# Kernel optimization log

Measured on AMD Instinct MI355X. Metric: run time of the kernel, lower is better.

The kernel has to match this reference:

```python
import jax, jax.numpy as jnp
import numpy as np

B, S, D = 1, 8192, 1024
H, HD = 16, 64
WIN = 1024      # sliding_window_size
CHUNK = 1024    # chunk_size
OVERLAP = 128   # chunk_overlap


def setup_inputs() -> dict:
    key = jax.random.key(0)
    ks = jax.random.split(key, 5)
    s = 1.0 / np.sqrt(D)
    inp = {"x": jax.random.normal(ks[0], (B, S, D), jnp.float32)}
    for i, n in enumerate(["Wq", "Wk", "Wv", "Wo"]):
        inp[n] = jax.random.normal(ks[1 + i], (D, D), jnp.float32) * s
    for n in ["bq", "bk", "bv", "bo"]:
        inp[n] = jnp.zeros((D,), jnp.float32)
    return inp


def _attend_chunk(q, k, v, chunk_start, win_start):
    # q: [B, Lq, H, HD]; k, v: [B, Lk, H, HD]
    Lq, Lk = q.shape[1], k.shape[1]
    q_abs = chunk_start + jnp.arange(Lq)[:, None]   # absolute query positions
    k_abs = win_start + jnp.arange(Lk)[None, :]     # absolute key positions
    allowed = (k_abs >= q_abs - WIN // 2) & (k_abs < q_abs + WIN // 2)
    scale = 1.0 / np.sqrt(HD)
    scores = jnp.einsum('bqhd,bkhd->bhqk', q, k) * scale  # [B,H,Lq,Lk]
    scores = jnp.where(allowed[None, None], scores, -jnp.inf)
    p = jax.nn.softmax(scores, axis=-1)
    return jnp.einsum('bhqk,bkhd->bqhd', p, v)


def _overlap_weight(cs, ce):
    # replicate torch linspace overlap-add blend weights (host-side constants)
    w = np.ones(ce - cs, np.float32)
    if cs > 0:
        n = min(cs + OVERLAP, ce) - cs
        w[:n] = np.linspace(0.0, 1.0, n, dtype=np.float32)
    if ce < S:
        os_ = max(cs, ce - OVERLAP)
        w[os_ - cs:] = np.linspace(1.0, 0.0, ce - os_, dtype=np.float32)
    return jnp.asarray(w)


def reference(x, Wq, bq, Wk, bk, Wv, bv, Wo, bo):
    q = (x @ Wq.T + bq).reshape(B, S, H, HD)
    k = (x @ Wk.T + bk).reshape(B, S, H, HD)
    v = (x @ Wv.T + bv).reshape(B, S, H, HD)
    out = jnp.zeros((B, S, H, HD), x.dtype)
    step = CHUNK - OVERLAP
    for cs in range(0, S, step):  # static Python loop over ~10 chunks
        ce = min(cs + CHUNK, S)
        ws, we = max(0, cs - WIN // 2), min(S, ce + WIN // 2)
        o = _attend_chunk(q[:, cs:ce], k[:, ws:we], v[:, ws:we], cs, ws)
        w = _overlap_weight(cs, ce)
        out = out.at[:, cs:ce].add(o * w[None, :, None, None])
    out = out.reshape(B, S, D)
    return out @ Wo.T + bo
```

## Files before the change

kernel.cpp:

```cpp
#include <hip/hip_runtime.h>

#define DEVI __device__ __forceinline__

constexpr int S = 8192, D = 1024, H = 16, HD = 64;
constexpr int NQKV = 3 * D;

typedef __attribute__((ext_vector_type(8))) __bf16 bf16x8;
typedef __attribute__((ext_vector_type(8))) unsigned short us8;
typedef __attribute__((ext_vector_type(4))) float f32x4;

DEVI unsigned short f2b(float f) {
  unsigned int u = __float_as_uint(f);
  u += 0x7fff + ((u >> 16) & 1);
  return (unsigned short)(u >> 16);
}

DEVI ushort4 cvt4(float4 v) {
  ushort4 r; r.x = f2b(v.x); r.y = f2b(v.y); r.z = f2b(v.z); r.w = f2b(v.w); return r;
}

DEVI void load_lds16(const void* g, void* l) {
  __builtin_amdgcn_global_load_lds((const __attribute__((address_space(1))) void*)g,
                                   (__attribute__((address_space(3))) void*)l,
                                   16, 0, 0);
}

__global__ void prep_kernel(const float4* __restrict__ x,
                            const float4* __restrict__ Wq, const float4* __restrict__ Wk,
                            const float4* __restrict__ Wv, const float4* __restrict__ Wo,
                            const float4* __restrict__ bq, const float4* __restrict__ bk,
                            const float4* __restrict__ bv,
                            ushort4* __restrict__ xb, ushort4* __restrict__ wqkv,
                            ushort4* __restrict__ wob, float4* __restrict__ biasq)
{
  constexpr int NX = S * D / 4;
  constexpr int NW = D * D / 4;
  constexpr int NB = D / 4;
  constexpr int TOT = NX + 4 * NW + 3 * NB;
  for (int i = blockIdx.x * blockDim.x + threadIdx.x; i < TOT; i += gridDim.x * blockDim.x) {
    if (i < NX) {
      xb[i] = cvt4(x[i]);
    } else if (i < NX + 3 * NW) {
      int j = i - NX;
      const float4* src = (j < NW) ? Wq : ((j < 2 * NW) ? Wk : Wv);
      int jj = (j < NW) ? j : ((j < 2 * NW) ? j - NW : j - 2 * NW);
      wqkv[j] = cvt4(src[jj]);
    } else if (i < NX + 4 * NW) {
      int j = i - NX - 3 * NW;
      wob[j] = cvt4(Wo[j]);
    } else {
      int j = i - NX - 4 * NW;
      const float4* src = (j < NB) ? bq : ((j < 2 * NB) ? bk : bv);
      int jj = (j < NB) ? j : ((j < 2 * NB) ? j - NB : j - 2 * NB);
      biasq[j] = src[jj];
    }
  }
}

template<int LDC, bool OUT_BF16>
__global__ __launch_bounds__(256)
void gemm_nt(const unsigned short* __restrict__ A,
             const unsigned short* __restrict__ B,
             const float* __restrict__ bias,
             void* __restrict__ C, int K)
{
  __shared__ __align__(16) unsigned short As[128 * 32];
  __shared__ __align__(16) unsigned short Bs[128 * 32];
  const int tid = threadIdx.x;
  const int wave = tid >> 6, lane = tid & 63;
  const int quad = lane >> 4, l15 = lane & 15;
  const int m0 = blockIdx.x * 128, n0 = blockIdx.y * 128;
  const int wr = wave >> 1, wc = wave & 1;

  const f32x4 fzero = {0.f, 0.f, 0.f, 0.f};
  f32x4 acc[4][4];
#pragma unroll
  for (int i = 0; i < 4; ++i)
#pragma unroll
    for (int j = 0; j < 4; ++j) acc[i][j] = fzero;

  const int segr = lane >> 2;
  const int cpst = lane & 3;

  for (int k0 = 0; k0 < K; k0 += 32) {
    __syncthreads();
#pragma unroll
    for (int j = 0; j < 4; ++j) {
      const int s = wave * 4 + j;
      const int s7 = s & 7;
      const int r = s7 * 16 + segr;
      const int c = cpst ^ ((r >> 1) & 3);
      const unsigned short* g = (s < 8)
        ? A + (size_t)(m0 + r) * K + k0 + c * 8
        : B + (size_t)(n0 + r) * K + k0 + c * 8;
      unsigned short* l = ((s < 8) ? As : Bs) + s7 * 512;
      load_lds16(g, l);
    }
    __syncthreads();

    bf16x8 af[4], bfr[4];
#pragma unroll
    for (int it = 0; it < 4; ++it) {
      const int r = wr * 64 + it * 16 + l15;
      const int cp = quad ^ ((r >> 1) & 3);
      af[it] = *(const bf16x8*)&As[r * 32 + cp * 8];
    }
#pragma unroll
    for (int jt = 0; jt < 4; ++jt) {
      const int r = wc * 64 + jt * 16 + l15;
      const int cp = quad ^ ((r >> 1) & 3);
      bfr[jt] = *(const bf16x8*)&Bs[r * 32 + cp * 8];
    }
#pragma unroll
    for (int it = 0; it < 4; ++it)
#pragma unroll
      for (int jt = 0; jt < 4; ++jt)
        acc[it][jt] = __builtin_amdgcn_mfma_f32_16x16x32_bf16(af[it], bfr[jt], acc[it][jt], 0, 0, 0);
  }

#pragma unroll
  for (int it = 0; it < 4; ++it)
#pragma unroll
    for (int jt = 0; jt < 4; ++jt) {
      const int col = n0 + wc * 64 + jt * 16 + l15;
      const float bv = bias[col];
#pragma unroll
      for (int i = 0; i < 4; ++i) {
        const int row = m0 + wr * 64 + it * 16 + quad * 4 + i;
        const float v = acc[it][jt][i] + bv;
        if constexpr (OUT_BF16)
          ((unsigned short*)C)[(size_t)row * LDC + col] = f2b(v);
        else
          ((float*)C)[(size_t)row * LDC + col] = v;
      }
    }
}

__global__ __launch_bounds__(256)
void attn_fused(const unsigned short* __restrict__ qkv,
                unsigned short* __restrict__ attnb)
{
  __shared__ __align__(16) unsigned short Ks[2][64 * 64];
  __shared__ __align__(16) unsigned short Vt[2][64 * 72];
  __shared__ __align__(16) unsigned short Ps[4][16 * 72];
  const int tid = threadIdx.x;
  const int wave = tid >> 6, lane = tid & 63;
  const int quad = lane >> 4, l15 = lane & 15;
  const int h = blockIdx.y;
  const int q0 = blockIdx.x * 128;
  const int wq0 = q0 + wave * 32;

  const unsigned short* Qp = qkv + h * HD;
  const unsigned short* Kp = qkv + D + h * HD;
  const unsigned short* Vp = qkv + 2 * D + h * HD;

  bf16x8 qf[2][2];
#pragma unroll
  for (int rt = 0; rt < 2; ++rt)
#pragma unroll
    for (int ksp = 0; ksp < 2; ++ksp)
      qf[rt][ksp] = *(const bf16x8*)(Qp + (size_t)(wq0 + rt * 16 + l15) * NQKV + ksp * 32 + quad * 8);

  const f32x4 fzero = {0.f, 0.f, 0.f, 0.f};
  f32x4 o[2][4];
  float lr[2][4];
#pragma unroll
  for (int rt = 0; rt < 2; ++rt)
#pragma unroll
    for (int i = 0; i < 4; ++i) { o[rt][i] = fzero; lr[rt][i] = 0.f; }

  const int ks = (q0 >= 512) ? (q0 - 512) : 0;
  const int ke = (q0 + 640 < S) ? (q0 + 640) : S;

  const int skey = tid >> 3;
  const int sg   = tid & 7;
  const int kdc  = sg ^ (skey & 7);

  us8 vreg[2];

#define STAGE_K(kt_, b_)                                                          \
  {                                                                               \
    _Pragma("unroll")                                                             \
    for (int r = 0; r < 2; ++r)                                                   \
      load_lds16(Kp + (size_t)((kt_) + skey + r * 32) * NQKV + kdc * 8,           \
                 &Ks[b_][(size_t)tid * 8 + r * 2048]);                            \
  }
#define LOAD_V(kt_)                                                               \
  {                                                                               \
    _Pragma("unroll")                                                             \
    for (int r = 0; r < 2; ++r)                                                   \
      vreg[r] = *(const us8*)(Vp + (size_t)((kt_) + skey + r * 32) * NQKV + sg * 8); \
  }
#define SCAT_V(b_)                                                                \
  {                                                                               \
    _Pragma("unroll")                                                             \
    for (int r = 0; r < 2; ++r) {                                                 \
      const int key = skey + r * 32;                                              \
      const int ch = (key >> 3) ^ sg;                                             \
      unsigned short* dst = &Vt[b_][sg * 8 * 72 + ch * 8 + (key & 7)];            \
      _Pragma("unroll")                                                           \
      for (int j = 0; j < 8; ++j) dst[j * 72] = vreg[r][j];                       \
    }                                                                             \
  }

  STAGE_K(ks, 0);
  LOAD_V(ks);
  SCAT_V(0);

  int b = 0;
  for (int kt = ks; kt < ke; kt += 64, b ^= 1) {
    __syncthreads();
    const int nx = kt + 64;
    const bool more = (nx < ke);
    if (more) { STAGE_K(nx, b ^ 1); LOAD_V(nx); }

    if (kt + 63 >= wq0 - 512 && kt <= wq0 + 542) {
      unsigned short* Pw = (unsigned short*)Ps[wave];
#pragma unroll
      for (int st = 0; st < 2; ++st) {
        const int C0 = kt + st * 32;
        if (!((C0 + 31 >= wq0 - 512) && (C0 <= wq0 + 16 + 526))) continue;

        bf16x8 kf[2][2];
#pragma unroll
        for (int hh2 = 0; hh2 < 2; ++hh2)
#pragma unroll
          for (int ksp = 0; ksp < 2; ++ksp)
            kf[hh2][ksp] = *(const bf16x8*)&Ks[b][((st * 2 + hh2) * 16 + l15) * 64
                                                  + ((ksp * 4 + quad) ^ (l15 & 7)) * 8];
        bf16x8 vf[4];
#pragma unroll
        for (int vt = 0; vt < 4; ++vt) {
          const int d = vt * 16 + l15;
          vf[vt] = *(const bf16x8*)&Vt[b][d * 72 + (((st * 4 + quad) ^ (d >> 3)) & 7) * 8];
        }

#pragma unroll
        for (int rt = 0; rt < 2; ++rt) {
          const int R = wq0 + rt * 16;
          if (!((C0 + 31 >= R - 512) && (C0 <= R + 526))) continue;

#pragma unroll
          for (int hh2 = 0; hh2 < 2; ++hh2) {
            const int C = C0 + hh2 * 16;
            const bool any  = (C + 15 >= R - 512) && (C <= R + 526);
            const bool full = (C >= R - 497) && (C <= R + 496);
            float p[4];
            if (!any) {
              p[0] = p[1] = p[2] = p[3] = 0.f;
            } else {
              f32x4 z = fzero;
              z = __builtin_amdgcn_mfma_f32_16x16x32_bf16(qf[rt][0], kf[hh2][0], z, 0, 0, 0);
              z = __builtin_amdgcn_mfma_f32_16x16x32_bf16(qf[rt][1], kf[hh2][1], z, 0, 0, 0);
              if (full) {
#pragma unroll
                for (int i = 0; i < 4; ++i) p[i] = __expf(z[i] * 0.125f);
              } else {
#pragma unroll
                for (int i = 0; i < 4; ++i) {
                  const int qa = R + quad * 4 + i;
                  const int ka = C + l15;
                  const unsigned u = (unsigned)(ka - qa + 512);
                  p[i] = (u < 1024u) ? __expf(z[i] * 0.125f) : 0.f;
                }
              }
            }
#pragma unroll
            for (int i = 0; i < 4; ++i) {
              lr[rt][i] += p[i];
              Pw[(quad * 4 + i) * 72 + st * 32 + hh2 * 16 + l15] = f2b(p[i]);
            }
          }
          asm volatile("s_waitcnt lgkmcnt(0)" ::: "memory");

          const bf16x8 pf = *(const bf16x8*)&Pw[l15 * 72 + (st * 4 + quad) * 8];
#pragma unroll
          for (int vt = 0; vt < 4; ++vt)
            o[rt][vt] = __builtin_amdgcn_mfma_f32_16x16x32_bf16(pf, vf[vt], o[rt][vt], 0, 0, 0);
        }
      }
    }

    if (more) SCAT_V(b ^ 1);
  }

#pragma unroll
  for (int rt = 0; rt < 2; ++rt)
#pragma unroll
    for (int i = 0; i < 4; ++i) {
      float l = lr[rt][i];
#pragma unroll
      for (int dd = 1; dd < 16; dd <<= 1) l += __shfl_xor(l, dd);
      const int qa = wq0 + rt * 16 + quad * 4 + i;
      const float w = (qa >= S - 128) ? (1.0f + (float)(qa - (S - 128)) * (1.0f / 127.0f)) : 1.0f;
      const float scl = w / l;
#pragma unroll
      for (int vt = 0; vt < 4; ++vt)
        attnb[(size_t)qa * D + h * HD + vt * 16 + l15] = f2b(o[rt][vt][i] * scl);
    }
#undef STAGE_K
#undef LOAD_V
#undef SCAT_V
}

extern "C" void kernel_launch(void* const* d_in, const int* in_sizes, int n_in,
                              void* d_out, int out_size, void* d_ws, size_t ws_size,
                              hipStream_t stream)
{
  const float* x  = (const float*)d_in[0];
  const float* Wq = (const float*)d_in[1];
  const float* Wk = (const float*)d_in[2];
  const float* Wv = (const float*)d_in[3];
  const float* Wo = (const float*)d_in[4];
  const float* bq = (const float*)d_in[5];
  const float* bk = (const float*)d_in[6];
  const float* bv = (const float*)d_in[7];
  const float* bo = (const float*)d_in[8];

  char* ws = (char*)d_ws;
  unsigned short* xb    = (unsigned short*)(ws);
  unsigned short* wqkv  = (unsigned short*)(ws + 16777216);
  unsigned short* wob   = (unsigned short*)(ws + 23068672);
  float*          biasq = (float*)         (ws + 25165824);
  unsigned short* qkv   = (unsigned short*)(ws + 25178112);
  unsigned short* attnb = (unsigned short*)(ws + 75509760);

  prep_kernel<<<2048, 256, 0, stream>>>((const float4*)x, (const float4*)Wq, (const float4*)Wk,
                                        (const float4*)Wv, (const float4*)Wo, (const float4*)bq,
                                        (const float4*)bk, (const float4*)bv,
                                        (ushort4*)xb, (ushort4*)wqkv, (ushort4*)wob, (float4*)biasq);

  gemm_nt<NQKV, true><<<dim3(64, 24), 256, 0, stream>>>(xb, wqkv, biasq, (void*)qkv, D);
  attn_fused<<<dim3(S / 128, H), 256, 0, stream>>>(qkv, attnb);
  gemm_nt<D, false><<<dim3(64, 8), 256, 0, stream>>>(attnb, wob, bo, d_out, D);
}
```

Before: 304.8 us.

## Compute transposed scores, read K from global, vectorize P stores

Measured after the change: 310.8 us. Within noise of the previous version (+2.0%).

```diff
diff --git a/kernel.cpp b/kernel.cpp
--- a/kernel.cpp
+++ b/kernel.cpp
@@ -6,6 +6,7 @@
 constexpr int NQKV = 3 * D;
 
 typedef __attribute__((ext_vector_type(8))) __bf16 bf16x8;
+typedef __attribute__((ext_vector_type(4))) __bf16 bf16x4;
 typedef __attribute__((ext_vector_type(8))) unsigned short us8;
 typedef __attribute__((ext_vector_type(4))) float f32x4;
 
@@ -19,7 +20,7 @@
   ushort4 r; r.x = f2b(v.x); r.y = f2b(v.y); r.z = f2b(v.z); r.w = f2b(v.w); return r;
 }
 
-DEVI void load_lds16(const void* g, void* l) {
+DEVI void load_lds16b(const void* g, void* l) {
   __builtin_amdgcn_global_load_lds((const __attribute__((address_space(1))) void*)g,
                                    (__attribute__((address_space(3))) void*)l,
                                    16, 0, 0);
@@ -94,7 +95,7 @@
         ? A + (size_t)(m0 + r) * K + k0 + c * 8
         : B + (size_t)(n0 + r) * K + k0 + c * 8;
       unsigned short* l = ((s < 8) ? As : Bs) + s7 * 512;
-      load_lds16(g, l);
+      load_lds16b(g, l);
     }
     __syncthreads();
 
@@ -140,9 +141,8 @@
 void attn_fused(const unsigned short* __restrict__ qkv,
                 unsigned short* __restrict__ attnb)
 {
-  __shared__ __align__(16) unsigned short Ks[2][64 * 64];
   __shared__ __align__(16) unsigned short Vt[2][64 * 72];
-  __shared__ __align__(16) unsigned short Ps[4][16 * 72];
+  __shared__ __align__(16) unsigned short Ps[4][16 * 40];
   const int tid = threadIdx.x;
   const int wave = tid >> 6, lane = tid & 63;
   const int quad = lane >> 4, l15 = lane & 15;
@@ -163,28 +163,20 @@
 
   const f32x4 fzero = {0.f, 0.f, 0.f, 0.f};
   f32x4 o[2][4];
-  float lr[2][4];
+  float lr[2] = {0.f, 0.f};
 #pragma unroll
   for (int rt = 0; rt < 2; ++rt)
 #pragma unroll
-    for (int i = 0; i < 4; ++i) { o[rt][i] = fzero; lr[rt][i] = 0.f; }
+    for (int vt = 0; vt < 4; ++vt) o[rt][vt] = fzero;
 
   const int ks = (q0 >= 512) ? (q0 - 512) : 0;
   const int ke = (q0 + 640 < S) ? (q0 + 640) : S;
 
   const int skey = tid >> 3;
   const int sg   = tid & 7;
-  const int kdc  = sg ^ (skey & 7);
 
   us8 vreg[2];
 
-#define STAGE_K(kt_, b_)                                                          \
-  {                                                                               \
-    _Pragma("unroll")                                                             \
-    for (int r = 0; r < 2; ++r)                                                   \
-      load_lds16(Kp + (size_t)((kt_) + skey + r * 32) * NQKV + kdc * 8,           \
-                 &Ks[b_][(size_t)tid * 8 + r * 2048]);                            \
-  }
 #define LOAD_V(kt_)                                                               \
   {                                                                               \
     _Pragma("unroll")                                                             \
@@ -203,31 +195,32 @@
     }                                                                             \
   }
 
-  STAGE_K(ks, 0);
   LOAD_V(ks);
   SCAT_V(0);
+
+  constexpr float L2E8 = 0.18033688011112042f;
 
   int b = 0;
   for (int kt = ks; kt < ke; kt += 64, b ^= 1) {
     __syncthreads();
     const int nx = kt + 64;
     const bool more = (nx < ke);
-    if (more) { STAGE_K(nx, b ^ 1); LOAD_V(nx); }
+    if (more) LOAD_V(nx);
 
     if (kt + 63 >= wq0 - 512 && kt <= wq0 + 542) {
       unsigned short* Pw = (unsigned short*)Ps[wave];
 #pragma unroll
       for (int st = 0; st < 2; ++st) {
         const int C0 = kt + st * 32;
-        if (!((C0 + 31 >= wq0 - 512) && (C0 <= wq0 + 16 + 526))) continue;
+        if (!((C0 + 31 >= wq0 - 512) && (C0 <= wq0 + 542))) continue;
 
         bf16x8 kf[2][2];
 #pragma unroll
         for (int hh2 = 0; hh2 < 2; ++hh2)
 #pragma unroll
           for (int ksp = 0; ksp < 2; ++ksp)
-            kf[hh2][ksp] = *(const bf16x8*)&Ks[b][((st * 2 + hh2) * 16 + l15) * 64
-                                                  + ((ksp * 4 + quad) ^ (l15 & 7)) * 8];
+            kf[hh2][ksp] = *(const bf16x8*)(Kp + (size_t)(C0 + hh2 * 16 + l15) * NQKV
+                                            + ksp * 32 + quad * 8);
         bf16x8 vf[4];
 #pragma unroll
         for (int vt = 0; vt < 4; ++vt) {
@@ -239,6 +232,7 @@
         for (int rt = 0; rt < 2; ++rt) {
           const int R = wq0 + rt * 16;
           if (!((C0 + 31 >= R - 512) && (C0 <= R + 526))) continue;
+          const int qa = R + l15;
 
 #pragma unroll
           for (int hh2 = 0; hh2 < 2; ++hh2) {
@@ -250,30 +244,23 @@
               p[0] = p[1] = p[2] = p[3] = 0.f;
             } else {
               f32x4 z = fzero;
-              z = __builtin_amdgcn_mfma_f32_16x16x32_bf16(qf[rt][0], kf[hh2][0], z, 0, 0, 0);
-              z = __builtin_amdgcn_mfma_f32_16x16x32_bf16(qf[rt][1], kf[hh2][1], z, 0, 0, 0);
+              z = __builtin_amdgcn_mfma_f32_16x16x32_bf16(kf[hh2][0], qf[rt][0], z, 0, 0, 0);
+              z = __builtin_amdgcn_mfma_f32_16x16x32_bf16(kf[hh2][1], qf[rt][1], z, 0, 0, 0);
               if (full) {
 #pragma unroll
-                for (int i = 0; i < 4; ++i) p[i] = __expf(z[i] * 0.125f);
+                for (int i = 0; i < 4; ++i) p[i] = __builtin_amdgcn_exp2f(z[i] * L2E8);
               } else {
-#pragma unroll
-                for (int i = 0; i < 4; ++i) {
-                  const int qa = R + quad * 4 + i;
-                  const int ka = C + l15;
-                  const unsigned u = (unsigned)(ka - qa + 512);
-                  p[i] = (u < 1024u) ? __expf(z[i] * 0.125f) : 0.f;
-                }
+                const int base = C + quad * 4 - qa + 512;
+#pragma unroll
+                for (int i = 0; i < 4; ++i)
+                  p[i] = ((unsigned)(base + i) < 1024u) ? __builtin_amdgcn_exp2f(z[i] * L2E8) : 0.f;
               }
             }
-#pragma unroll
-            for (int i = 0; i < 4; ++i) {
-              lr[rt][i] += p[i];
-              Pw[(quad * 4 + i) * 72 + st * 32 + hh2 * 16 + l15] = f2b(p[i]);
-            }
+            lr[rt] += p[0] + p[1] + p[2] + p[3];
+            f32x4 pv = {p[0], p[1], p[2], p[3]};
+            *(bf16x4*)&Pw[l15 * 40 + hh2 * 16 + quad * 4] = __builtin_convertvector(pv, bf16x4);
           }
-          asm volatile("s_waitcnt lgkmcnt(0)" ::: "memory");
-
-          const bf16x8 pf = *(const bf16x8*)&Pw[l15 * 72 + (st * 4 + quad) * 8];
+          const bf16x8 pf = *(const bf16x8*)&Pw[l15 * 40 + quad * 8];
 #pragma unroll
           for (int vt = 0; vt < 4; ++vt)
             o[rt][vt] = __builtin_amdgcn_mfma_f32_16x16x32_bf16(pf, vf[vt], o[rt][vt], 0, 0, 0);
@@ -284,21 +271,26 @@
     if (more) SCAT_V(b ^ 1);
   }
 
+  float lt[2];
+#pragma unroll
+  for (int rt = 0; rt < 2; ++rt) {
+    float l = lr[rt];
+    l += __shfl_xor(l, 16);
+    l += __shfl_xor(l, 32);
+    lt[rt] = l;
+  }
 #pragma unroll
   for (int rt = 0; rt < 2; ++rt)
 #pragma unroll
     for (int i = 0; i < 4; ++i) {
-      float l = lr[rt][i];
-#pragma unroll
-      for (int dd = 1; dd < 16; dd <<= 1) l += __shfl_xor(l, dd);
+      const float lq = __shfl(lt[rt], quad * 4 + i);
       const int qa = wq0 + rt * 16 + quad * 4 + i;
       const float w = (qa >= S - 128) ? (1.0f + (float)(qa - (S - 128)) * (1.0f / 127.0f)) : 1.0f;
-      const float scl = w / l;
+      const float scl = w / lq;
 #pragma unroll
       for (int vt = 0; vt < 4; ++vt)
-        attnb[(size_t)qa * D + h * HD + vt * 16 + l15] = f2b(o[rt][vt][i] * scl);
-    }
-#undef STAGE_K
+        ((__bf16*)attnb)[(size_t)qa * D + h * HD + vt * 16 + l15] = (__bf16)(o[rt][vt][i] * scl);
+    }
 #undef LOAD_V
 #undef SCAT_V
 }
```
